# Kernel optimization log

Measured on AMD Instinct MI355X. Metric: run time of the kernel, lower is better.

## Reference

```python
import jax, jax.numpy as jnp
import numpy as np

HEADS = 16
HIDDEN = 1024
D_HEAD = HIDDEN // HEADS
SCALE = float(D_HEAD) ** 0.5


def setup_inputs() -> dict:
    key = jax.random.key(0)
    ks = jax.random.split(key, 11)
    B, L = 2, 2048
    x = jax.random.normal(ks[0], (B, L, HIDDEN), dtype=jnp.float32)
    # 0/1 padding mask, broadcast over heads and query positions
    mask = jax.random.randint(ks[1], (B, 1, 1, L), 0, 2).astype(jnp.float32)
    s = 1.0 / np.sqrt(HIDDEN)
    Wq = jax.random.normal(ks[2], (HIDDEN, HIDDEN), dtype=jnp.float32) * s
    bq = jax.random.normal(ks[3], (HIDDEN,), dtype=jnp.float32) * s
    Wk = jax.random.normal(ks[4], (HIDDEN, HIDDEN), dtype=jnp.float32) * s
    bk = jax.random.normal(ks[5], (HIDDEN,), dtype=jnp.float32) * s
    Wv = jax.random.normal(ks[6], (HIDDEN, HIDDEN), dtype=jnp.float32) * s
    bv = jax.random.normal(ks[7], (HIDDEN,), dtype=jnp.float32) * s
    Wo = jax.random.normal(ks[8], (HIDDEN, HIDDEN), dtype=jnp.float32) * s
    bo = jax.random.normal(ks[9], (HIDDEN,), dtype=jnp.float32) * s
    return {"x": x, "mask": mask, "Wq": Wq, "bq": bq, "Wk": Wk, "bk": bk,
            "Wv": Wv, "bv": bv, "Wo": Wo, "bo": bo}


def reference(x, mask, Wq, bq, Wk, bk, Wv, bv, Wo, bo):
    B, L, _ = x.shape
    # projections (Linear: x @ W + b), split heads -> [B, H, L, Dh]
    def proj(W, b):
        return (jnp.dot(x, W) + b).reshape(B, L, HEADS, D_HEAD).transpose(0, 2, 1, 3)
    q = proj(Wq, bq)
    k = proj(Wk, bk)
    v = proj(Wv, bv)
    # scaled dot-product with additive mask: scores [B, H, Lq, Lk]
    scores = jnp.einsum('bhqd,bhkd->bhqk', q, k) / SCALE + mask * (-10000.0)
    attn = jax.nn.softmax(scores, axis=-1)  # dropout p=0.0 -> identity
    out = jnp.einsum('bhqk,bhkd->bhqd', attn, v)
    out = out.transpose(0, 2, 1, 3).reshape(B, L, HIDDEN)
    return jnp.dot(out, Wo) + bo
```

## Files before the change

### kernel.cpp

```cpp
#include <hip/hip_runtime.h>
#include <math.h>

typedef unsigned short u16;
typedef short v8s __attribute__((ext_vector_type(8)));
typedef float v4f __attribute__((ext_vector_type(4)));

#define HIDDEN 1024
#define L_SEQ 2048
#define NH 16
#define DH 64
#define NKMAX 1280

#define QSCALE 0.18033688011112042f

__device__ __forceinline__ u16 f2bf(float f) {
  union { float f; unsigned int i; } c; c.f = f;
  unsigned int x = c.i;
  unsigned int r = (x + 0x7fffu + ((x >> 16) & 1u)) >> 16;
  return (u16)r;
}

#if defined(__has_builtin)
#if __has_builtin(__builtin_amdgcn_cvt_pk_bf16_f32)
#define HAS_PKBF 1
#endif
#if __has_builtin(__builtin_amdgcn_exp2f)
#define EXP2(x) __builtin_amdgcn_exp2f(x)
#endif
#if __has_builtin(__builtin_amdgcn_rcpf)
#define RCP(x) __builtin_amdgcn_rcpf(x)
#endif
#endif
#ifndef EXP2
#define EXP2(x) exp2f(x)
#endif
#ifndef RCP
#define RCP(x) (1.0f / (x))
#endif

__device__ __forceinline__ unsigned pkbf(float a, float b) {
#ifdef HAS_PKBF
  typedef __bf16 v2bf __attribute__((ext_vector_type(2)));
  union { v2bf v; unsigned u; } c;
  c.v = __builtin_amdgcn_cvt_pk_bf16_f32(a, b);
  return c.u;
#else
  return (unsigned)f2bf(a) | ((unsigned)f2bf(b) << 16);
#endif
}

__device__ __forceinline__ void gload16(const void* g, void* l) {
  void* gg = const_cast<void*>(g);
  __builtin_amdgcn_global_load_lds(
      (__attribute__((address_space(1))) void*)gg,
      (__attribute__((address_space(3))) void*)l, 16, 0, 0);
}

__global__ __launch_bounds__(256) void prep(
    const float* __restrict__ x, u16* __restrict__ xb,
    const float* __restrict__ Wq, const float* __restrict__ Wk,
    const float* __restrict__ Wv, const float* __restrict__ Wo,
    u16* __restrict__ WtQ, u16* __restrict__ WtK,
    u16* __restrict__ WtV, u16* __restrict__ WtO,
    const float* __restrict__ maskg, u16* __restrict__ keep,
    unsigned* __restrict__ nkslot) {
  const int bid = blockIdx.x;
  const int t = threadIdx.x;

  if (bid < 2048) {
    const int i = (bid * 256 + t) * 8;
    const float4 a = *(const float4*)(x + i);
    const float4 b = *(const float4*)(x + i + 4);
    unsigned o[4] = {pkbf(a.x, a.y), pkbf(a.z, a.w), pkbf(b.x, b.y), pkbf(b.z, b.w)};
    *(uint4*)(xb + i) = *(const uint4*)o;
    return;
  }

  if (bid < 6144) {
    const int m = bid - 2048;
    const int z = m >> 10;
    const int rem = m & 1023;
    const int bx = rem & 31, by = rem >> 5;
    const float* src; u16* dst;
    if (z == 0) { src = Wq; dst = WtQ; }
    else if (z == 1) { src = Wk; dst = WtK; }
    else if (z == 2) { src = Wv; dst = WtV; }
    else { src = Wo; dst = WtO; }

    __shared__ u16 tile[32][33];
    const int tx = t & 31, ty = t >> 5;
    const int xcol = bx * 32 + tx;
    const int y0 = by * 32;
#pragma unroll
    for (int i = ty; i < 32; i += 8)
      tile[i][tx] = f2bf(src[(size_t)(y0 + i) * HIDDEN + xcol]);
    __syncthreads();
    const int xo = y0 + tx;
#pragma unroll
    for (int i = ty; i < 32; i += 8)
      dst[(size_t)(bx * 32 + i) * HIDDEN + xo] = tile[tx][i];
    return;
  }

  if (t < 64) {
    const int b = bid - 6144;
    const int lane = t;
    const float* mp = maskg + b * L_SEQ;
    int cnt = 0;
#pragma unroll 1
    for (int j = 0; j < 32; ++j) cnt += (mp[lane * 32 + j] == 0.0f) ? 1 : 0;
    int inc = cnt;
#pragma unroll
    for (int off = 1; off < 64; off <<= 1) {
      const int v = __shfl_up(inc, off, 64);
      if (lane >= off) inc += v;
    }
    int base = inc - cnt;
    u16* kp = keep + b * L_SEQ;
#pragma unroll 1
    for (int j = 0; j < 32; ++j) {
      const int k = lane * 32 + j;
      if (mp[k] == 0.0f) kp[base++] = (u16)k;
    }
    const int total = __shfl(inc, 63, 64);
    for (int i = total + lane; i < NKMAX; i += 64) kp[i] = 0;
    if (lane == 0) nkslot[b] = (unsigned)total;
  }
}

__global__ __launch_bounds__(256) void gemm128(
    const u16* __restrict__ A,
    const u16* __restrict__ B0, const u16* __restrict__ B1, const u16* __restrict__ B2,
    const float* __restrict__ bias0, const float* __restrict__ bias1, const float* __restrict__ bias2,
    u16* __restrict__ C0, u16* __restrict__ C1, u16* __restrict__ C2,
    float* __restrict__ Cf, const u16* __restrict__ keep,
    const unsigned* __restrict__ nkslot,
    int qkv_mode) {
  __shared__ __align__(16) u16 As[128 * 32];
  __shared__ __align__(16) u16 Bs[128 * 32];

  const u16* Bt; const float* bias; u16* C;
  if (blockIdx.z == 0) { Bt = B0; bias = bias0; C = C0; }
  else if (blockIdx.z == 1) { Bt = B1; bias = bias1; C = C1; }
  else { Bt = B2; bias = bias2; C = C2; }
  const int mode = qkv_mode ? (blockIdx.z == 0 ? 1 : (blockIdx.z == 1 ? 2 : 3)) : 0;
  const float oscale = (mode == 1) ? QSCALE : 1.0f;

  const int t = threadIdx.x;
  const int lane = t & 63;
  const int wave = t >> 6;
  const int quad = lane >> 4;
  const int l16 = lane & 15;
  const int wm = wave >> 1;
  const int wn = wave & 1;

  const int n0 = blockIdx.x * 128;
  const int sr = t >> 2;
  const int sc = (t & 3) * 8;

  int m0 = blockIdx.y * 128;
  int kvb = 0;
  const u16* Ag0;
  const u16* Ag1;
  if (mode == 2 || mode == 3) {
    const int y = blockIdx.y;
    if (y >= 20) return;
    kvb = y / 10;
    m0 = (y % 10) * 128;
    const unsigned nk = nkslot[kvb];
    if ((unsigned)m0 >= ((nk + 63u) & ~63u)) return;
    const int sr0 = keep[kvb * L_SEQ + m0 + sr];
    const int sr1 = keep[kvb * L_SEQ + m0 + 64 + sr];
    Ag0 = A + ((size_t)(kvb * L_SEQ + sr0)) * HIDDEN + sc;
    Ag1 = A + ((size_t)(kvb * L_SEQ + sr1)) * HIDDEN + sc;
  } else {
    Ag0 = A + (size_t)(m0 + sr) * HIDDEN + sc;
    Ag1 = Ag0 + (size_t)64 * HIDDEN;
  }
  const u16* Bg0 = Bt + (size_t)(n0 + sr) * HIDDEN + sc;
  const u16* Bg1 = Bg0 + (size_t)64 * HIDDEN;
  u16* Al0 = &As[sr * 32 + sc];
  u16* Al1 = &As[(64 + sr) * 32 + sc];
  u16* Bl0 = &Bs[sr * 32 + sc];
  u16* Bl1 = &Bs[(64 + sr) * 32 + sc];

  v4f acc[4][4];
#pragma unroll
  for (int mi = 0; mi < 4; ++mi)
#pragma unroll
    for (int ni = 0; ni < 4; ++ni)
      acc[mi][ni] = (v4f){0.f, 0.f, 0.f, 0.f};

  for (int k0 = 0; k0 < HIDDEN; k0 += 32) {
    __syncthreads();
    gload16(Ag0 + k0, Al0);
    gload16(Ag1 + k0, Al1);
    gload16(Bg0 + k0, Bl0);
    gload16(Bg1 + k0, Bl1);
    __syncthreads();

    v8s a[4], b[4];
#pragma unroll
    for (int mi = 0; mi < 4; ++mi)
      a[mi] = *(const v8s*)&As[(wm * 64 + mi * 16 + l16) * 32 + quad * 8];
#pragma unroll
    for (int ni = 0; ni < 4; ++ni)
      b[ni] = *(const v8s*)&Bs[(wn * 64 + ni * 16 + l16) * 32 + quad * 8];
#pragma unroll
    for (int mi = 0; mi < 4; ++mi)
#pragma unroll
      for (int ni = 0; ni < 4; ++ni)
        acc[mi][ni] = __builtin_amdgcn_mfma_f32_16x16x32_bf16(a[mi], b[ni], acc[mi][ni], 0, 0, 0);
  }

#pragma unroll
  for (int ni = 0; ni < 4; ++ni) {
    const int col = n0 + wn * 64 + ni * 16 + l16;
    const float bv = bias[col];
#pragma unroll
    for (int mi = 0; mi < 4; ++mi) {
      const int row0 = m0 + wm * 64 + mi * 16 + quad * 4;
      const float v0 = (acc[mi][ni][0] + bv) * oscale;
      const float v1 = (acc[mi][ni][1] + bv) * oscale;
      const float v2 = (acc[mi][ni][2] + bv) * oscale;
      const float v3 = (acc[mi][ni][3] + bv) * oscale;
      if (mode == 0) {
        Cf[(size_t)(row0 + 0) * HIDDEN + col] = v0;
        Cf[(size_t)(row0 + 1) * HIDDEN + col] = v1;
        Cf[(size_t)(row0 + 2) * HIDDEN + col] = v2;
        Cf[(size_t)(row0 + 3) * HIDDEN + col] = v3;
      } else if (mode == 1) {
        const int hh = col >> 6, d = col & 63;
        const float vv[4] = {v0, v1, v2, v3};
#pragma unroll
        for (int i = 0; i < 4; ++i) {
          const int rr = row0 + i;
          const int bb = rr >> 11, l = rr & 2047;
          C[((size_t)(bb * NH + hh) * L_SEQ + l) * DH + d] = f2bf(vv[i]);
        }
      } else if (mode == 2) {
        const int hh = col >> 6, d = col & 63;
        const float vv[4] = {v0, v1, v2, v3};
#pragma unroll
        for (int i = 0; i < 4; ++i)
          C[((size_t)(kvb * NH + hh) * L_SEQ + row0 + i) * DH + d] = f2bf(vv[i]);
      } else {
        const int hh = col >> 6, d = col & 63;
        unsigned pk[2] = {pkbf(v0, v1), pkbf(v2, v3)};
        *(uint2*)&C[((size_t)((kvb * NH + hh) * DH + d)) * L_SEQ + row0] = *(const uint2*)pk;
      }
    }
  }
}

__global__ __launch_bounds__(256) void attn64(
    const u16* __restrict__ Qg, const u16* __restrict__ Kcg, const u16* __restrict__ VTg,
    const unsigned* __restrict__ nkslot, u16* __restrict__ Og) {
  __shared__ __align__(16) u16 lds[20480];

  const int t = threadIdx.x;
  const int lane = t & 63;
  const int w = t >> 6;
  const int quad = lane >> 4;
  const int l16 = lane & 15;
  const int e7 = l16 & 7;

  const int q0 = blockIdx.x * 64;
  const int bh = blockIdx.y;
  const int b = bh >> 4;
  const int h = bh & 15;

  const size_t base = (size_t)bh * L_SEQ * DH;
  const u16* Qp = Qg + base;
  const u16* Kp = Kcg + base;
  const u16* VTp = VTg + base;

  const int nkb = (int)nkslot[b];
  const int ntiles = (nkb + 63) >> 6;

  const int r8 = lane >> 3;
  const int sl = lane & 7;
  const int og8 = (sl ^ r8) * 8;
  const int koff = (w * 16 + r8) * DH + og8;
  const int voff = (w * 16 + r8) * L_SEQ + og8;

  gload16(Kp + koff, &lds[(w * 16) * 64]);
  gload16(Kp + koff + 8 * DH, &lds[(w * 16 + 8) * 64]);
  gload16(VTp + voff, &lds[8192 + (w * 16) * 64]);
  gload16(VTp + voff + 8 * L_SEQ, &lds[8192 + (w * 16 + 8) * 64]);

  {
    const int r = t >> 3, oc = t & 7;
    *(uint4*)&lds[16384 + r * 64 + ((oc ^ (r & 7)) * 8)] =
        *(const uint4*)&Qp[(size_t)(q0 + r) * DH + oc * 8];
    const int r2 = r + 32;
    *(uint4*)&lds[16384 + r2 * 64 + ((oc ^ (r2 & 7)) * 8)] =
        *(const uint4*)&Qp[(size_t)(q0 + r2) * DH + oc * 8];
  }
  __syncthreads();

  const int rowq = 16384 + (w * 16 + l16) * 64;
  const v8s qf0 = *(const v8s*)&lds[rowq + ((quad ^ e7) * 8)];
  const v8s qf1 = *(const v8s*)&lds[rowq + (((4 + quad) ^ e7) * 8)];

  const v8s ones = {0x3F80, 0x3F80, 0x3F80, 0x3F80, 0x3F80, 0x3F80, 0x3F80, 0x3F80};
  v8s of0 = ones, of1 = ones;

  v4f o[4], o4 = (v4f){0.f, 0.f, 0.f, 0.f};
#pragma unroll
  for (int ti = 0; ti < 4; ++ti) o[ti] = (v4f){0.f, 0.f, 0.f, 0.f};

  for (int n = 0; n < ntiles; ++n) {
    __syncthreads();
    const int ksb = (n & 1) * 4096;
    const int vtb = 8192 + (n & 1) * 4096;
    if (n + 1 < ntiles) {
      const int k1 = (n + 1) * 64;
      const int ksb2 = ((n + 1) & 1) * 4096;
      const int vtb2 = 8192 + ((n + 1) & 1) * 4096;
      gload16(Kp + (size_t)k1 * DH + koff, &lds[ksb2 + (w * 16) * 64]);
      gload16(Kp + (size_t)k1 * DH + koff + 8 * DH, &lds[ksb2 + (w * 16 + 8) * 64]);
      gload16(VTp + voff + k1, &lds[vtb2 + (w * 16) * 64]);
      gload16(VTp + voff + k1 + 8 * L_SEQ, &lds[vtb2 + (w * 16 + 8) * 64]);
    }
    const int k0 = n * 64;
    if (k0 + 64 > nkb) {
      for (int e = t; e < 4096; e += 256) {
        const int lr = e >> 6;
        if (k0 + lr >= nkb) lds[ksb + e] = 0;
      }
      for (int e = t; e < 4096; e += 256) {
        const int d = e >> 6, cc = e & 63;
        if (k0 + cc >= nkb)
          lds[vtb + d * 64 + (((cc >> 3) ^ (d & 7)) * 8) + (cc & 7)] = 0;
      }
#pragma unroll
      for (int j = 0; j < 8; ++j) {
        ((short*)&of0)[j] = (k0 + quad * 8 + j < nkb) ? (short)0x3F80 : (short)0;
        ((short*)&of1)[j] = (k0 + 32 + quad * 8 + j < nkb) ? (short)0x3F80 : (short)0;
      }
      __syncthreads();
    }

#pragma unroll
    for (int ni = 0; ni < 4; ++ni) {
      const int rowk = ksb + (ni * 16 + l16) * 64;
      const v8s kf0 = *(const v8s*)&lds[rowk + ((quad ^ e7) * 8)];
      const v8s kf1 = *(const v8s*)&lds[rowk + (((4 + quad) ^ e7) * 8)];
      v4f s = (v4f){0.f, 0.f, 0.f, 0.f};
      s = __builtin_amdgcn_mfma_f32_16x16x32_bf16(kf0, qf0, s, 0, 0, 0);
      s = __builtin_amdgcn_mfma_f32_16x16x32_bf16(kf1, qf1, s, 0, 0, 0);
      const float p0 = EXP2(s[0]);
      const float p1 = EXP2(s[1]);
      const float p2 = EXP2(s[2]);
      const float p3 = EXP2(s[3]);
      const int slo = rowq + (((ni * 2 + (quad >> 1)) ^ e7) * 8) + (quad & 1) * 4;
      unsigned pk2[2] = {pkbf(p0, p1), pkbf(p2, p3)};
      *(uint2*)&lds[slo] = *(const uint2*)pk2;
    }

    const v8s pf0 = *(const v8s*)&lds[rowq + ((quad ^ e7) * 8)];
    const v8s pf1 = *(const v8s*)&lds[rowq + (((4 + quad) ^ e7) * 8)];

    o4 = __builtin_amdgcn_mfma_f32_16x16x32_bf16(pf0, of0, o4, 0, 0, 0);
    o4 = __builtin_amdgcn_mfma_f32_16x16x32_bf16(pf1, of1, o4, 0, 0, 0);

#pragma unroll
    for (int ti = 0; ti < 4; ++ti) {
      const int rowv = vtb + (ti * 16 + l16) * 64;
      const v8s vf0 = *(const v8s*)&lds[rowv + ((quad ^ e7) * 8)];
      const v8s vf1 = *(const v8s*)&lds[rowv + (((4 + quad) ^ e7) * 8)];
      o[ti] = __builtin_amdgcn_mfma_f32_16x16x32_bf16(pf0, vf0, o[ti], 0, 0, 0);
      o[ti] = __builtin_amdgcn_mfma_f32_16x16x32_bf16(pf1, vf1, o[ti], 0, 0, 0);
    }
  }

  float linv[4];
#pragma unroll
  for (int i = 0; i < 4; ++i) linv[i] = RCP(o4[i]);

#pragma unroll
  for (int ti = 0; ti < 4; ++ti) {
#pragma unroll
    for (int i = 0; i < 4; ++i) {
      const int q = q0 + w * 16 + quad * 4 + i;
      const int d = ti * 16 + l16;
      Og[(size_t)(b * L_SEQ + q) * HIDDEN + h * DH + d] = f2bf(o[ti][i] * linv[i]);
    }
  }
}

extern "C" void kernel_launch(void* const* d_in, const int* in_sizes, int n_in,
                              void* d_out, int out_size, void* d_ws, size_t ws_size,
                              hipStream_t stream) {
  const float* x    = (const float*)d_in[0];
  const float* mask = (const float*)d_in[1];
  const float* Wq   = (const float*)d_in[2];
  const float* bq   = (const float*)d_in[3];
  const float* Wk   = (const float*)d_in[4];
  const float* bk   = (const float*)d_in[5];
  const float* Wv   = (const float*)d_in[6];
  const float* bv   = (const float*)d_in[7];
  const float* Wo   = (const float*)d_in[8];
  const float* bo   = (const float*)d_in[9];
  float* out = (float*)d_out;
  u16* ws = (u16*)d_ws;

  const unsigned M1 = 1u << 20;
  u16* WtQ = ws;
  u16* WtK = ws + M1;
  u16* WtV = ws + 2 * M1;
  u16* WtO = ws + 3 * M1;
  u16* xb  = ws + 4 * M1;
  u16* Qb  = ws + 8 * M1;
  u16* Kc  = ws + 12 * M1;
  u16* VTc = ws + 16 * M1;
  u16* Ob  = ws + 20 * M1;
  u16* keep = ws + 16 * M1 - 8192;
  unsigned* nkslot = (unsigned*)(ws + 16 * M1 - 8192 - 8);

  prep<<<6146, 256, 0, stream>>>(x, xb, Wq, Wk, Wv, Wo, WtQ, WtK, WtV, WtO,
                                 mask, keep, nkslot);
  gemm128<<<dim3(8, 32, 3), 256, 0, stream>>>(xb, WtQ, WtK, WtV, bq, bk, bv,
                                              Qb, Kc, VTc, nullptr, keep, nkslot, 1);
  attn64<<<dim3(32, 32), 256, 0, stream>>>(Qb, Kc, VTc, nkslot, Ob);
  gemm128<<<dim3(8, 32, 1), 256, 0, stream>>>(Ob, WtO, WtO, WtO, bo, bo, bo,
                                              nullptr, nullptr, nullptr, out, nullptr, nullptr, 0);
}
```

Baseline: 192.0 us.

## Rewrite attention with 32x32 MFMA, 128-query tiles, register-resident probabilities

Replaces the 64-query attention kernel with one that gives each wave 32 query rows and uses 32x32x16 bf16 MFMA for both QK^T and PV. The probabilities are packed to bf16 and exchanged between wave halves with shuffles instead of a round trip through LDS. The row sum is accumulated in registers instead of through an extra MFMA against a ones vector, and masking of the tail tile is done by zeroing probabilities instead of zeroing LDS with an extra barrier. The aim is to double K/V tile reuse per block and cut LDS traffic and barriers. It costs more registers per thread and halves the grid, which may lower occupancy.

New measurement: 191.7 us. About the same (-0.1%).

```diff
diff --git a/kernel.cpp b/kernel.cpp
--- a/kernel.cpp
+++ b/kernel.cpp
@@ -4,6 +4,7 @@
 typedef unsigned short u16;
 typedef short v8s __attribute__((ext_vector_type(8)));
 typedef float v4f __attribute__((ext_vector_type(4)));
+typedef float v16f __attribute__((ext_vector_type(16)));
 
 #define HIDDEN 1024
 #define L_SEQ 2048
@@ -54,6 +55,13 @@
   __builtin_amdgcn_global_load_lds(
       (__attribute__((address_space(1))) void*)gg,
       (__attribute__((address_space(3))) void*)l, 16, 0, 0);
+}
+
+__device__ __forceinline__ v16f vzero16() {
+  v16f z;
+#pragma unroll
+  for (int i = 0; i < 16; ++i) z[i] = 0.f;
+  return z;
 }
 
 __global__ __launch_bounds__(256) void prep(
@@ -253,19 +261,37 @@
   }
 }
 
-__global__ __launch_bounds__(256) void attn64(
+
+#define MKPF(dst, P0, P1, P2, P3, P4, P5, P6, P7)                   \
+  {                                                                 \
+    const unsigned a_ = pkbf(P0, P1), c_ = pkbf(P2, P3);            \
+    const unsigned b_ = pkbf(P4, P5), d_ = pkbf(P6, P7);            \
+    const unsigned a2_ = (unsigned)__shfl((int)a_, lane ^ 32, 64);  \
+    const unsigned b2_ = (unsigned)__shfl((int)b_, lane ^ 32, 64);  \
+    const unsigned c2_ = (unsigned)__shfl((int)c_, lane ^ 32, 64);  \
+    const unsigned d2_ = (unsigned)__shfl((int)d_, lane ^ 32, 64);  \
+    union { unsigned u[4]; v8s v; } f_;                             \
+    f_.u[0] = lo32 ? a_ : b2_;                                      \
+    f_.u[1] = lo32 ? c_ : d2_;                                      \
+    f_.u[2] = lo32 ? a2_ : b_;                                      \
+    f_.u[3] = lo32 ? c2_ : d_;                                      \
+    dst = f_.v;                                                     \
+  }
+
+__global__ __launch_bounds__(256) void attn128(
     const u16* __restrict__ Qg, const u16* __restrict__ Kcg, const u16* __restrict__ VTg,
     const unsigned* __restrict__ nkslot, u16* __restrict__ Og) {
-  __shared__ __align__(16) u16 lds[20480];
+  __shared__ __align__(16) u16 lds[16384];
 
   const int t = threadIdx.x;
   const int lane = t & 63;
   const int w = t >> 6;
-  const int quad = lane >> 4;
-  const int l16 = lane & 15;
-  const int e7 = l16 & 7;
-
-  const int q0 = blockIdx.x * 64;
+  const int l31 = lane & 31;
+  const int hi = lane >> 5;
+  const bool lo32 = lane < 32;
+  const int e7 = l31 & 7;
+
+  const int q0 = blockIdx.x * 128;
   const int bh = blockIdx.y;
   const int b = bh >> 4;
   const int h = bh & 15;
@@ -289,26 +315,14 @@
   gload16(VTp + voff, &lds[8192 + (w * 16) * 64]);
   gload16(VTp + voff + 8 * L_SEQ, &lds[8192 + (w * 16 + 8) * 64]);
 
-  {
-    const int r = t >> 3, oc = t & 7;
-    *(uint4*)&lds[16384 + r * 64 + ((oc ^ (r & 7)) * 8)] =
-        *(const uint4*)&Qp[(size_t)(q0 + r) * DH + oc * 8];
-    const int r2 = r + 32;
-    *(uint4*)&lds[16384 + r2 * 64 + ((oc ^ (r2 & 7)) * 8)] =
-        *(const uint4*)&Qp[(size_t)(q0 + r2) * DH + oc * 8];
-  }
-  __syncthreads();
-
-  const int rowq = 16384 + (w * 16 + l16) * 64;
-  const v8s qf0 = *(const v8s*)&lds[rowq + ((quad ^ e7) * 8)];
-  const v8s qf1 = *(const v8s*)&lds[rowq + (((4 + quad) ^ e7) * 8)];
-
-  const v8s ones = {0x3F80, 0x3F80, 0x3F80, 0x3F80, 0x3F80, 0x3F80, 0x3F80, 0x3F80};
-  v8s of0 = ones, of1 = ones;
-
-  v4f o[4], o4 = (v4f){0.f, 0.f, 0.f, 0.f};
-#pragma unroll
-  for (int ti = 0; ti < 4; ++ti) o[ti] = (v4f){0.f, 0.f, 0.f, 0.f};
+  const int qrow = q0 + w * 32 + l31;
+  v8s qf[4];
+#pragma unroll
+  for (int dc = 0; dc < 4; ++dc)
+    qf[dc] = *(const v8s*)&Qp[(size_t)qrow * DH + dc * 16 + hi * 8];
+
+  v16f oacc0 = vzero16(), oacc1 = vzero16();
+  float lsum = 0.f;
 
   for (int n = 0; n < ntiles; ++n) {
     __syncthreads();
@@ -323,70 +337,69 @@
       gload16(VTp + voff + k1, &lds[vtb2 + (w * 16) * 64]);
       gload16(VTp + voff + k1 + 8 * L_SEQ, &lds[vtb2 + (w * 16 + 8) * 64]);
     }
-    const int k0 = n * 64;
-    if (k0 + 64 > nkb) {
-      for (int e = t; e < 4096; e += 256) {
-        const int lr = e >> 6;
-        if (k0 + lr >= nkb) lds[ksb + e] = 0;
+
+    v16f s0 = vzero16(), s1 = vzero16();
+#pragma unroll
+    for (int dc = 0; dc < 4; ++dc) {
+      const int po = ((dc * 2 + hi) ^ e7) * 8;
+      const v8s kf0 = *(const v8s*)&lds[ksb + l31 * 64 + po];
+      const v8s kf1 = *(const v8s*)&lds[ksb + (32 + l31) * 64 + po];
+      s0 = __builtin_amdgcn_mfma_f32_32x32x16_bf16(kf0, qf[dc], s0, 0, 0, 0);
+      s1 = __builtin_amdgcn_mfma_f32_32x32x16_bf16(kf1, qf[dc], s1, 0, 0, 0);
+    }
+
+    const int kb0 = n * 64;
+    float p[32];
+#pragma unroll
+    for (int r = 0; r < 16; ++r) {
+      p[r]      = EXP2(s0[r]);
+      p[16 + r] = EXP2(s1[r]);
+    }
+    if (kb0 + 64 > nkb) {
+#pragma unroll
+      for (int r = 0; r < 16; ++r) {
+        const int kk = kb0 + (r & 3) + 8 * (r >> 2) + 4 * hi;
+        if (kk >= nkb) p[r] = 0.f;
+        if (kk + 32 >= nkb) p[16 + r] = 0.f;
       }
-      for (int e = t; e < 4096; e += 256) {
-        const int d = e >> 6, cc = e & 63;
-        if (k0 + cc >= nkb)
-          lds[vtb + d * 64 + (((cc >> 3) ^ (d & 7)) * 8) + (cc & 7)] = 0;
+    }
+    {
+      float a0 = 0.f, a1 = 0.f, a2 = 0.f, a3 = 0.f;
+#pragma unroll
+      for (int r = 0; r < 8; ++r) {
+        a0 += p[r]; a1 += p[8 + r]; a2 += p[16 + r]; a3 += p[24 + r];
       }
-#pragma unroll
-      for (int j = 0; j < 8; ++j) {
-        ((short*)&of0)[j] = (k0 + quad * 8 + j < nkb) ? (short)0x3F80 : (short)0;
-        ((short*)&of1)[j] = (k0 + 32 + quad * 8 + j < nkb) ? (short)0x3F80 : (short)0;
-      }
-      __syncthreads();
-    }
-
-#pragma unroll
-    for (int ni = 0; ni < 4; ++ni) {
-      const int rowk = ksb + (ni * 16 + l16) * 64;
-      const v8s kf0 = *(const v8s*)&lds[rowk + ((quad ^ e7) * 8)];
-      const v8s kf1 = *(const v8s*)&lds[rowk + (((4 + quad) ^ e7) * 8)];
-      v4f s = (v4f){0.f, 0.f, 0.f, 0.f};
-      s = __builtin_amdgcn_mfma_f32_16x16x32_bf16(kf0, qf0, s, 0, 0, 0);
-      s = __builtin_amdgcn_mfma_f32_16x16x32_bf16(kf1, qf1, s, 0, 0, 0);
-      const float p0 = EXP2(s[0]);
-      const float p1 = EXP2(s[1]);
-      const float p2 = EXP2(s[2]);
-      const float p3 = EXP2(s[3]);
-      const int slo = rowq + (((ni * 2 + (quad >> 1)) ^ e7) * 8) + (quad & 1) * 4;
-      unsigned pk2[2] = {pkbf(p0, p1), pkbf(p2, p3)};
-      *(uint2*)&lds[slo] = *(const uint2*)pk2;
-    }
-
-    const v8s pf0 = *(const v8s*)&lds[rowq + ((quad ^ e7) * 8)];
-    const v8s pf1 = *(const v8s*)&lds[rowq + (((4 + quad) ^ e7) * 8)];
-
-    o4 = __builtin_amdgcn_mfma_f32_16x16x32_bf16(pf0, of0, o4, 0, 0, 0);
-    o4 = __builtin_amdgcn_mfma_f32_16x16x32_bf16(pf1, of1, o4, 0, 0, 0);
-
-#pragma unroll
-    for (int ti = 0; ti < 4; ++ti) {
-      const int rowv = vtb + (ti * 16 + l16) * 64;
-      const v8s vf0 = *(const v8s*)&lds[rowv + ((quad ^ e7) * 8)];
-      const v8s vf1 = *(const v8s*)&lds[rowv + (((4 + quad) ^ e7) * 8)];
-      o[ti] = __builtin_amdgcn_mfma_f32_16x16x32_bf16(pf0, vf0, o[ti], 0, 0, 0);
-      o[ti] = __builtin_amdgcn_mfma_f32_16x16x32_bf16(pf1, vf1, o[ti], 0, 0, 0);
-    }
-  }
-
-  float linv[4];
-#pragma unroll
-  for (int i = 0; i < 4; ++i) linv[i] = RCP(o4[i]);
-
-#pragma unroll
-  for (int ti = 0; ti < 4; ++ti) {
-#pragma unroll
-    for (int i = 0; i < 4; ++i) {
-      const int q = q0 + w * 16 + quad * 4 + i;
-      const int d = ti * 16 + l16;
-      Og[(size_t)(b * L_SEQ + q) * HIDDEN + h * DH + d] = f2bf(o[ti][i] * linv[i]);
-    }
+      lsum += (a0 + a1) + (a2 + a3);
+    }
+
+    v8s pf0, pf1, pf2, pf3;
+    MKPF(pf0, p[0],  p[1],  p[2],  p[3],  p[4],  p[5],  p[6],  p[7]);
+    MKPF(pf1, p[8],  p[9],  p[10], p[11], p[12], p[13], p[14], p[15]);
+    MKPF(pf2, p[16], p[17], p[18], p[19], p[20], p[21], p[22], p[23]);
+    MKPF(pf3, p[24], p[25], p[26], p[27], p[28], p[29], p[30], p[31]);
+
+#pragma unroll
+    for (int kc = 0; kc < 4; ++kc) {
+      const v8s pb = (kc == 0) ? pf0 : (kc == 1) ? pf1 : (kc == 2) ? pf2 : pf3;
+      const int po = ((kc * 2 + hi) ^ e7) * 8;
+      const v8s vf0 = *(const v8s*)&lds[vtb + l31 * 64 + po];
+      const v8s vf1 = *(const v8s*)&lds[vtb + (32 + l31) * 64 + po];
+      oacc0 = __builtin_amdgcn_mfma_f32_32x32x16_bf16(vf0, pb, oacc0, 0, 0, 0);
+      oacc1 = __builtin_amdgcn_mfma_f32_32x32x16_bf16(vf1, pb, oacc1, 0, 0, 0);
+    }
+  }
+
+  const float ltot = lsum + __shfl(lsum, lane ^ 32, 64);
+  const float linv = RCP(ltot);
+
+  const size_t ob = ((size_t)(b * L_SEQ + qrow)) * HIDDEN + h * DH;
+#pragma unroll
+  for (int r = 0; r < 16; r += 2) {
+    const int d0 = (r & 3) + 8 * (r >> 2) + 4 * hi;
+    const unsigned w0 = pkbf(oacc0[r] * linv, oacc0[r + 1] * linv);
+    const unsigned w1 = pkbf(oacc1[r] * linv, oacc1[r + 1] * linv);
+    *(unsigned*)&Og[ob + d0] = w0;
+    *(unsigned*)&Og[ob + 32 + d0] = w1;
   }
 }
 
@@ -423,7 +436,7 @@
                                  mask, keep, nkslot);
   gemm128<<<dim3(8, 32, 3), 256, 0, stream>>>(xb, WtQ, WtK, WtV, bq, bk, bv,
                                               Qb, Kc, VTc, nullptr, keep, nkslot, 1);
-  attn64<<<dim3(32, 32), 256, 0, stream>>>(Qb, Kc, VTc, nkslot, Ob);
+  attn128<<<dim3(16, 32), 256, 0, stream>>>(Qb, Kc, VTc, nkslot, Ob);
   gemm128<<<dim3(8, 32, 1), 256, 0, stream>>>(Ob, WtO, WtO, WtO, bo, bo, bo,
                                               nullptr, nullptr, nullptr, out, nullptr, nullptr, 0);
 }
```
